# Performance work log

Hardware: AMD Instinct MI355X
Metric: run time of the kernel (lower is better)

## Reference

```python
import jax, jax.numpy as jnp
import numpy as np

N = 120000   # hits
K = 512      # non-noise objects (ids 1..K; id 0 = noise)
D = 8        # cluster-space dim
C = 6        # pid classes
Q_MIN = 1.0
NOISE_THR = 0
PAYLOAD_W = 1.0
EPS = 1e-9


def setup_inputs() -> dict:
    key = jax.random.key(0)
    ks = jax.random.split(key, 9)
    beta = jax.random.uniform(ks[0], (N,), dtype=jnp.float32) * 0.95 + 0.01  # keep arctanh finite
    x = jax.random.normal(ks[1], (N, D), dtype=jnp.float32)
    object_id = jax.random.randint(ks[2], (N,), 0, K + 1).astype(jnp.int32)
    # guarantee every object id (and noise id 0) appears at least once
    object_id = object_id.at[: K + 1].set(jnp.arange(K + 1, dtype=jnp.int32))
    energy = jax.random.normal(ks[3], (N,), dtype=jnp.float32)
    energy_per_hit = jax.random.normal(ks[4], (N,), dtype=jnp.float32)
    momentum = jax.random.normal(ks[5], (N, 3), dtype=jnp.float32)
    momentum_per_hit = jax.random.normal(ks[6], (N, 3), dtype=jnp.float32)
    pid_logits = jax.random.normal(ks[7], (N, C), dtype=jnp.float32)
    pid_per_hit = jax.random.randint(ks[8], (N,), 0, C).astype(jnp.int32)
    return dict(beta=beta, x=x, object_id=object_id, energy=energy,
                energy_per_hit=energy_per_hit, momentum=momentum,
                momentum_per_hit=momentum_per_hit, pid_logits=pid_logits,
                pid_per_hit=pid_per_hit)


def _oc_core(beta, x, object_id):
    """condensation_loss_tiger with weights=1, max_n_rep=0 (no repulsive sampling)."""
    oids = jnp.arange(1, K + 1, dtype=object_id.dtype)
    att_mask = object_id[:, None] == oids[None, :]              # [N, K]
    q = jnp.arctanh(beta) ** 2 + Q_MIN                          # [N]
    alphas = jnp.argmax(q[:, None] * att_mask, axis=0)          # [K] condensation points
    x_k = x[alphas]                                             # [K, D]
    q_k = q[alphas]                                             # [K]
    # squared euclidean distance via gemm (avoids [N,K,D] intermediate)
    d2 = (jnp.sum(x * x, axis=1)[:, None] + jnp.sum(x_k * x_k, axis=1)[None, :]
          - 2.0 * (x @ x_k.T))
    d2 = jnp.maximum(d2, 0.0)                                   # [N, K]
    dist = jnp.sqrt(jnp.maximum(d2, 1e-12))
    qw = q[:, None] * q_k[None, :]                              # [N, K]
    # attractive: per-object normalized by hits in object, then mean over objects
    att_norm = jnp.sum(att_mask, axis=0).astype(x.dtype)        # [K]
    v_att = jnp.sum(jnp.where(att_mask, qw * d2, 0.0) / (att_norm + EPS)[None, :]) / K
    # repulsive: hinge (1 - dist), normalized by n_hits not in object
    rep_mask = (~att_mask) & (dist < 1.0)
    n_rep_k = jnp.sum(~att_mask, axis=0).astype(x.dtype)        # [K]
    n_rep = jnp.sum(rep_mask)
    v_rep = jnp.sum(jnp.where(rep_mask, qw * (1.0 - dist), 0.0) / (n_rep_k + EPS)[None, :]) / K
    l_coward = jnp.mean(1.0 - beta[alphas])
    noise_m = (object_id <= NOISE_THR).astype(beta.dtype)
    l_noise = jnp.sum(beta * noise_m) / jnp.sum(noise_m)
    return v_att, v_rep, l_coward, l_noise, n_rep


def reference(beta, x, object_id, energy, energy_per_hit, momentum,
              momentum_per_hit, pid_logits, pid_per_hit):
    v_att, v_rep, l_coward, l_noise, n_rep = _oc_core(beta, x, object_id)
    oc_total = v_att + v_rep + l_coward + l_noise
    # payload losses on non-noise hits (masked means == F.*_loss on gathered rows)
    m = (object_id > NOISE_THR).astype(beta.dtype)              # [N]
    nm = jnp.sum(m)
    e_loss = jnp.sum((energy - energy_per_hit) ** 2 * m) / nm
    p_loss = jnp.sum((momentum - momentum_per_hit) ** 2 * m[:, None]) / (nm * momentum.shape[1])
    logp = jax.nn.log_softmax(pid_logits, axis=-1)              # [N, C]
    nll = -jnp.take_along_axis(logp, pid_per_hit[:, None], axis=1)[:, 0]
    pid_loss = jnp.sum(nll * m) / nm
    total = oc_total + PAYLOAD_W * (e_loss + p_loss + pid_loss)
    return (v_att, v_rep, l_coward, l_noise, n_rep.astype(jnp.float32),
            oc_total, e_loss, p_loss, pid_loss, total)
```

## Files before the change

kernel.cpp:

```cpp
#include <hip/hip_runtime.h>
#include <math.h>

#define KOBJ 512
#define KTW 8
#define TK 32
#define NTILE (KOBJ / TK)
#define HB 8
#define HCH (256 * HB)
#define MPREP 512
#define GGATH 16

typedef _Float16 half2_t __attribute__((ext_vector_type(2)));

__device__ __forceinline__ float wave_red_f(float v) {
  #pragma unroll
  for (int off = 32; off > 0; off >>= 1) v += __shfl_down(v, off, 64);
  return v;
}

__device__ __forceinline__ float q_of_beta(float b) {
  float a = 0.5f * __logf((1.f + b) / (1.f - b));
  return fmaf(a, a, 1.f);
}

__device__ __forceinline__ float dot8h(uint4 kx, const uint* y, float acc) {
#if __has_builtin(__builtin_amdgcn_fdot2)
  acc = __builtin_amdgcn_fdot2(__builtin_bit_cast(half2_t, y[0]),
                               __builtin_bit_cast(half2_t, kx.x), acc, false);
  acc = __builtin_amdgcn_fdot2(__builtin_bit_cast(half2_t, y[1]),
                               __builtin_bit_cast(half2_t, kx.y), acc, false);
  acc = __builtin_amdgcn_fdot2(__builtin_bit_cast(half2_t, y[2]),
                               __builtin_bit_cast(half2_t, kx.z), acc, false);
  acc = __builtin_amdgcn_fdot2(__builtin_bit_cast(half2_t, y[3]),
                               __builtin_bit_cast(half2_t, kx.w), acc, false);
#else
  const uint kk[4] = {kx.x, kx.y, kx.z, kx.w};
  #pragma unroll
  for (int c = 0; c < 4; c++) {
    half2_t a = __builtin_bit_cast(half2_t, y[c]);
    half2_t b = __builtin_bit_cast(half2_t, kk[c]);
    acc = fmaf((float)a.x, (float)b.x, acc);
    acc = fmaf((float)a.y, (float)b.y, acc);
  }
#endif
  return acc;
}

__global__ __launch_bounds__(256) void
k_prep(const float* __restrict__ beta, const int* __restrict__ oid,
       const float* __restrict__ energy, const float* __restrict__ eph,
       const float* __restrict__ mom, const float* __restrict__ mph,
       const float* __restrict__ logits, const int* __restrict__ pid,
       unsigned long long* __restrict__ amax_part,
       unsigned* __restrict__ cnt_part,
       float* __restrict__ scal_part, int n) {
  __shared__ unsigned long long lmax[KOBJ];
  __shared__ unsigned lcnt[KOBJ];
  for (int t = threadIdx.x; t < KOBJ; t += 256) { lmax[t] = 0ull; lcnt[t] = 0u; }
  __syncthreads();

  float e_t = 0.f, p_t = 0.f, pid_t = 0.f, noise_t = 0.f, ncnt = 0.f, mcnt = 0.f;
  for (int i = blockIdx.x * 256 + threadIdx.x; i < n; i += MPREP * 256) {
    float b = beta[i];
    int o = oid[i];
    if (o > 0) {
      float q = q_of_beta(b);
      unsigned long long key = ((unsigned long long)__float_as_uint(q) << 32)
                             | (unsigned long long)(unsigned)(~(unsigned)i);
      atomicMax(&lmax[o - 1], key);
      atomicAdd(&lcnt[o - 1], 1u);
      mcnt += 1.f;
      float de = energy[i] - eph[i];
      e_t = fmaf(de, de, e_t);
      float p0 = mom[3*i+0] - mph[3*i+0];
      float p1 = mom[3*i+1] - mph[3*i+1];
      float p2 = mom[3*i+2] - mph[3*i+2];
      p_t = fmaf(p0, p0, p_t); p_t = fmaf(p1, p1, p_t); p_t = fmaf(p2, p2, p_t);
      const float* lg = logits + 6*i;
      float l0=lg[0], l1=lg[1], l2=lg[2], l3=lg[3], l4=lg[4], l5=lg[5];
      float mx = fmaxf(fmaxf(fmaxf(l0,l1),fmaxf(l2,l3)), fmaxf(l4,l5));
      float s = __expf(l0-mx)+__expf(l1-mx)+__expf(l2-mx)
              + __expf(l3-mx)+__expf(l4-mx)+__expf(l5-mx);
      int pc = pid[i];
      float lp = (pc==0)?l0:(pc==1)?l1:(pc==2)?l2:(pc==3)?l3:(pc==4)?l4:l5;
      pid_t += mx + __logf(s) - lp;
    } else {
      noise_t += b;
      ncnt += 1.f;
    }
  }
  __syncthreads();

  for (int t = threadIdx.x; t < KOBJ; t += 256) {
    amax_part[(size_t)blockIdx.x * KOBJ + t] = lmax[t];
    cnt_part[(size_t)blockIdx.x * KOBJ + t]  = lcnt[t];
  }

  float vals[6] = {e_t, p_t, pid_t, noise_t, ncnt, mcnt};
  #pragma unroll
  for (int j = 0; j < 6; j++) vals[j] = wave_red_f(vals[j]);
  __shared__ float sred[4][6];
  int w = threadIdx.x >> 6, l = threadIdx.x & 63;
  if (l == 0) {
    #pragma unroll
    for (int j = 0; j < 6; j++) sred[w][j] = vals[j];
  }
  __syncthreads();
  if (threadIdx.x == 0) {
    #pragma unroll
    for (int j = 0; j < 6; j++)
      scal_part[blockIdx.x * 8 + j] = sred[0][j]+sred[1][j]+sred[2][j]+sred[3][j];
  }
}

__global__ __launch_bounds__(256) void
k_gather(const float* __restrict__ x, const float* __restrict__ beta,
         const unsigned long long* __restrict__ amax_part,
         const unsigned* __restrict__ cnt_part,
         uint* __restrict__ ktab, float* __restrict__ cow_part, int n) {
  int ko = threadIdx.x & 31;
  int chunk = threadIdx.x >> 5;
  int k = blockIdx.x * 32 + ko;
  const int mpc = MPREP / 8;
  int m0 = chunk * mpc, m1 = m0 + mpc;

  unsigned long long key = 0ull;
  unsigned cnt = 0u;
  for (int m = m0; m < m1; m++) {
    unsigned long long km = amax_part[(size_t)m * KOBJ + k];
    key = (km > key) ? km : key;
    cnt += cnt_part[(size_t)m * KOBJ + k];
  }
  __shared__ unsigned long long skey[8][32];
  __shared__ unsigned scnt[8][32];
  skey[chunk][ko] = key;
  scnt[chunk][ko] = cnt;
  __syncthreads();

  float cow = 0.f;
  if (chunk == 0) {
    #pragma unroll
    for (int c = 1; c < 8; c++) {
      unsigned long long kc = skey[c][ko];
      key = (kc > key) ? kc : key;
      cnt += scnt[c][ko];
    }
    unsigned idx = ~(unsigned)(key & 0xffffffffull);
    float q_k = __uint_as_float((unsigned)(key >> 32));
    const float4* xp = (const float4*)x;
    float4 xa = xp[2 * (size_t)idx];
    float4 xb = xp[2 * (size_t)idx + 1];
    float xv[8] = {xa.x, xa.y, xa.z, xa.w, xb.x, xb.y, xb.z, xb.w};
    float s2 = 0.f;
    #pragma unroll
    for (int c = 0; c < 8; c++) s2 = fmaf(xv[c], xv[c], s2);
    uint* kt = ktab + (size_t)k * KTW;
    #pragma unroll
    for (int c = 0; c < 4; c++) {
      half2_t hp = { (_Float16)xv[2*c], (_Float16)xv[2*c+1] };
      kt[c] = __builtin_bit_cast(uint, hp);
    }
    kt[4] = __float_as_uint(s2);
    kt[5] = __float_as_uint(q_k / ((float)(n - (int)cnt) + 1e-9f));
    kt[6] = __float_as_uint(q_k / ((float)cnt + 1e-9f));
    kt[7] = 0u;
    cow = 1.f - beta[idx];
  }
  cow = wave_red_f(cow);
  if (threadIdx.x == 0) cow_part[blockIdx.x] = cow;
}

__global__ __launch_bounds__(256, 4) void
k_pairs(const float* __restrict__ x, const float* __restrict__ beta,
        const int* __restrict__ oid, const uint* __restrict__ ktab,
        float* __restrict__ pairs_part, int n) {
  __shared__ __align__(16) uint skt[TK * KTW];
  const int tid = threadIdx.x;
  const int tile0 = blockIdx.y * TK;
  const int hbase = blockIdx.x * HCH;

  for (int t = tid; t < TK * KTW; t += 256)
    skt[t] = ktab[(size_t)tile0 * KTW + t];
  __syncthreads();

  uint yh[HB][4];
  float thr[HB], bh[HB], qi[HB];
  int own[HB];
  const float4* xp = (const float4*)x;
  #pragma unroll
  for (int h = 0; h < HB; h++) {
    int i = hbase + h * 256 + tid;
    if (i < n) {
      float4 xa = xp[2 * (size_t)i];
      float4 xb = xp[2 * (size_t)i + 1];
      float xi[8] = {xa.x, xa.y, xa.z, xa.w, xb.x, xb.y, xb.z, xb.w};
      float s = 0.f;
      #pragma unroll
      for (int c = 0; c < 8; c++) s = fmaf(xi[c], xi[c], s);
      bh[h] = s;
      thr[h] = 1.f - s;
      #pragma unroll
      for (int c = 0; c < 4; c++) {
        half2_t hy = { (_Float16)(-2.f * xi[2*c]), (_Float16)(-2.f * xi[2*c+1]) };
        yh[h][c] = __builtin_bit_cast(uint, hy);
      }
      qi[h] = q_of_beta(beta[i]);
      own[h] = oid[i] - 1 - tile0;
    } else {
      #pragma unroll
      for (int c = 0; c < 4; c++) yh[h][c] = 0u;
      bh[h] = 0.f;
      thr[h] = -1e30f;
      qi[h] = 0.f;
      own[h] = -1;
    }
  }

  float att = 0.f, rep = 0.f, nrep = 0.f;
  #pragma unroll 2
  for (int k = 0; k < TK; k++) {
    const uint* kr = &skt[k * KTW];
    uint4 kx = *(const uint4*)kr;
    float s2 = __uint_as_float(kr[4]);
    float wr = __uint_as_float(kr[5]);
    #pragma unroll
    for (int h = 0; h < HB; h++) {
      float dp = dot8h(kx, yh[h], s2);
      if (dp < thr[h]) {
        float d2 = dp + bh[h];
        float dist = sqrtf(fmaxf(d2, 1e-12f));
        rep = fmaf(qi[h] * (1.f - dist), wr, rep);
        nrep += 1.f;
      }
    }
  }

  #pragma unroll
  for (int h = 0; h < HB; h++) {
    int ko = own[h];
    if (ko >= 0 && ko < TK) {
      const uint* kr = &skt[ko * KTW];
      uint4 kx = *(const uint4*)kr;
      float s2 = __uint_as_float(kr[4]);
      float wr = __uint_as_float(kr[5]);
      float wa = __uint_as_float(kr[6]);
      float dp = dot8h(kx, yh[h], s2);
      float d2 = dp + bh[h];
      att = fmaf(qi[h] * fmaxf(d2, 0.f), wa, att);
      if (dp < thr[h]) {
        float dist = sqrtf(fmaxf(d2, 1e-12f));
        rep = fmaf(-qi[h] * (1.f - dist), wr, rep);
        nrep -= 1.f;
      }
    }
  }

  att = wave_red_f(att);
  rep = wave_red_f(rep);
  nrep = wave_red_f(nrep);
  __shared__ float sred[4][3];
  int w = tid >> 6, l = tid & 63;
  if (l == 0) { sred[w][0] = att; sred[w][1] = rep; sred[w][2] = nrep; }
  __syncthreads();
  if (tid == 0) {
    int bid = blockIdx.y * gridDim.x + blockIdx.x;
    pairs_part[bid * 4 + 0] = sred[0][0]+sred[1][0]+sred[2][0]+sred[3][0];
    pairs_part[bid * 4 + 1] = sred[0][1]+sred[1][1]+sred[2][1]+sred[3][1];
    pairs_part[bid * 4 + 2] = sred[0][2]+sred[1][2]+sred[2][2]+sred[3][2];
  }
}

__global__ __launch_bounds__(256) void
k_finalize(const float* __restrict__ pairs_part, int nblk_tot,
           const float* __restrict__ scal_part,
           const float* __restrict__ cow_part, float* __restrict__ out) {
  float v[9] = {0,0,0,0,0,0,0,0,0};
  for (int b = threadIdx.x; b < nblk_tot; b += 256) {
    v[0] += pairs_part[b * 4 + 0];
    v[1] += pairs_part[b * 4 + 1];
    v[2] += pairs_part[b * 4 + 2];
  }
  for (int m = threadIdx.x; m < MPREP; m += 256) {
    #pragma unroll
    for (int j = 0; j < 6; j++) v[3 + j] += scal_part[m * 8 + j];
  }
  #pragma unroll
  for (int j = 0; j < 9; j++) v[j] = wave_red_f(v[j]);
  __shared__ float sred[4][9];
  int w = threadIdx.x >> 6, l = threadIdx.x & 63;
  if (l == 0) {
    #pragma unroll
    for (int j = 0; j < 9; j++) sred[w][j] = v[j];
  }
  __syncthreads();
  if (threadIdx.x == 0) {
    float t[9];
    #pragma unroll
    for (int j = 0; j < 9; j++) t[j] = sred[0][j]+sred[1][j]+sred[2][j]+sred[3][j];
    float cow = 0.f;
    #pragma unroll
    for (int g = 0; g < GGATH; g++) cow += cow_part[g];
    float v_att  = t[0] / (float)KOBJ;
    float v_rep  = t[1] / (float)KOBJ;
    float n_rep  = t[2];
    float l_cow  = cow / (float)KOBJ;
    float l_noise = t[6] / t[7];
    float oc = v_att + v_rep + l_cow + l_noise;
    float nm = t[8];
    float e_loss  = t[3] / nm;
    float p_loss  = t[4] / (nm * 3.f);
    float pid_loss = t[5] / nm;
    out[0] = v_att;
    out[1] = v_rep;
    out[2] = l_cow;
    out[3] = l_noise;
    out[4] = n_rep;
    out[5] = oc;
    out[6] = e_loss;
    out[7] = p_loss;
    out[8] = pid_loss;
    out[9] = oc + e_loss + p_loss + pid_loss;
  }
}

extern "C" void kernel_launch(void* const* d_in, const int* in_sizes, int n_in,
                              void* d_out, int out_size, void* d_ws, size_t ws_size,
                              hipStream_t stream) {
  const float* beta   = (const float*)d_in[0];
  const float* x      = (const float*)d_in[1];
  const int*   oid    = (const int*)d_in[2];
  const float* energy = (const float*)d_in[3];
  const float* eph    = (const float*)d_in[4];
  const float* mom    = (const float*)d_in[5];
  const float* mph    = (const float*)d_in[6];
  const float* logits = (const float*)d_in[7];
  const int*   pid    = (const int*)d_in[8];
  float* out = (float*)d_out;
  const int n = in_sizes[0];
  const int nhb = (n + HCH - 1) / HCH;
  const int nblk_tot = nhb * NTILE;

  char* base = (char*)d_ws;
  size_t off = 0;
  uint*  ktab       = (uint*)(base + off);  off += (size_t)KOBJ * KTW * 4;
  float* cow_part   = (float*)(base + off); off += GGATH * 4;
  float* pairs_part = (float*)(base + off); off += (size_t)nblk_tot * 4 * 4;
  off = (off + 255) & ~(size_t)255;
  unsigned long long* amax_part = (unsigned long long*)(base + off); off += (size_t)MPREP * KOBJ * 8;
  unsigned* cnt_part = (unsigned*)(base + off);                      off += (size_t)MPREP * KOBJ * 4;
  float* scal_part   = (float*)(base + off);                         off += (size_t)MPREP * 8 * 4;

  k_prep<<<MPREP, 256, 0, stream>>>(beta, oid, energy, eph, mom, mph, logits, pid,
                                    amax_part, cnt_part, scal_part, n);
  k_gather<<<GGATH, 256, 0, stream>>>(x, beta, amax_part, cnt_part, ktab, cow_part, n);
  k_pairs<<<dim3(nhb, NTILE), 256, 0, stream>>>(x, beta, oid, ktab, pairs_part, n);
  k_finalize<<<1, 256, 0, stream>>>(pairs_part, nblk_tot, scal_part, cow_part, out);
}
```

Before: 114.7 us.

## Fuse gather, pairs and finalize into one kernel with last-block reduction

Removes the separate gather and finalize launches. Each pairs block now reduces the per-block argmax and count partials for its own object tile and builds the tile table in shared memory. The last block to finish, found through an atomic counter, does the final reduction. The prep grid is cut to 128 blocks so that each main block has fewer partials to reduce, at the cost of less parallelism in prep. Every main block now repeats the tile's partial reduction, which adds redundant global reads.

```diff
diff --git a/kernel.cpp b/kernel.cpp
--- a/kernel.cpp
+++ b/kernel.cpp
@@ -7,10 +7,12 @@
 #define NTILE (KOBJ / TK)
 #define HB 8
 #define HCH (256 * HB)
-#define MPREP 512
-#define GGATH 16
+#define MPREP 128
 
 typedef _Float16 half2_t __attribute__((ext_vector_type(2)));
+
+#define AGS(p, v) __hip_atomic_store((p), (v), __ATOMIC_RELAXED, __HIP_MEMORY_SCOPE_AGENT)
+#define AGL(p)    __hip_atomic_load((p), __ATOMIC_RELAXED, __HIP_MEMORY_SCOPE_AGENT)
 
 __device__ __forceinline__ float wave_red_f(float v) {
   #pragma unroll
@@ -53,9 +55,11 @@
        const float* __restrict__ logits, const int* __restrict__ pid,
        unsigned long long* __restrict__ amax_part,
        unsigned* __restrict__ cnt_part,
-       float* __restrict__ scal_part, int n) {
+       float* __restrict__ scal_part,
+       unsigned* __restrict__ done_cnt, int n) {
   __shared__ unsigned long long lmax[KOBJ];
   __shared__ unsigned lcnt[KOBJ];
+  if (blockIdx.x == 0 && threadIdx.x == 0) *done_cnt = 0u;
   for (int t = threadIdx.x; t < KOBJ; t += 256) { lmax[t] = 0ull; lcnt[t] = 0u; }
   __syncthreads();
 
@@ -113,78 +117,76 @@
   }
 }
 
-__global__ __launch_bounds__(256) void
-k_gather(const float* __restrict__ x, const float* __restrict__ beta,
-         const unsigned long long* __restrict__ amax_part,
-         const unsigned* __restrict__ cnt_part,
-         uint* __restrict__ ktab, float* __restrict__ cow_part, int n) {
-  int ko = threadIdx.x & 31;
-  int chunk = threadIdx.x >> 5;
-  int k = blockIdx.x * 32 + ko;
-  const int mpc = MPREP / 8;
-  int m0 = chunk * mpc, m1 = m0 + mpc;
-
-  unsigned long long key = 0ull;
-  unsigned cnt = 0u;
-  for (int m = m0; m < m1; m++) {
-    unsigned long long km = amax_part[(size_t)m * KOBJ + k];
-    key = (km > key) ? km : key;
-    cnt += cnt_part[(size_t)m * KOBJ + k];
-  }
+__global__ __launch_bounds__(256, 4) void
+k_main(const float* __restrict__ x, const float* __restrict__ beta,
+       const int* __restrict__ oid,
+       const unsigned long long* __restrict__ amax_part,
+       const unsigned* __restrict__ cnt_part,
+       const float* __restrict__ scal_part,
+       float* __restrict__ cow_part, float* __restrict__ pairs_part,
+       unsigned* __restrict__ done_cnt, float* __restrict__ out, int n) {
+  __shared__ __align__(16) uint skt[TK * KTW];
   __shared__ unsigned long long skey[8][32];
-  __shared__ unsigned scnt[8][32];
-  skey[chunk][ko] = key;
-  scnt[chunk][ko] = cnt;
-  __syncthreads();
-
-  float cow = 0.f;
-  if (chunk == 0) {
-    #pragma unroll
-    for (int c = 1; c < 8; c++) {
-      unsigned long long kc = skey[c][ko];
-      key = (kc > key) ? kc : key;
-      cnt += scnt[c][ko];
-    }
-    unsigned idx = ~(unsigned)(key & 0xffffffffull);
-    float q_k = __uint_as_float((unsigned)(key >> 32));
-    const float4* xp = (const float4*)x;
-    float4 xa = xp[2 * (size_t)idx];
-    float4 xb = xp[2 * (size_t)idx + 1];
-    float xv[8] = {xa.x, xa.y, xa.z, xa.w, xb.x, xb.y, xb.z, xb.w};
-    float s2 = 0.f;
-    #pragma unroll
-    for (int c = 0; c < 8; c++) s2 = fmaf(xv[c], xv[c], s2);
-    uint* kt = ktab + (size_t)k * KTW;
-    #pragma unroll
-    for (int c = 0; c < 4; c++) {
-      half2_t hp = { (_Float16)xv[2*c], (_Float16)xv[2*c+1] };
-      kt[c] = __builtin_bit_cast(uint, hp);
-    }
-    kt[4] = __float_as_uint(s2);
-    kt[5] = __float_as_uint(q_k / ((float)(n - (int)cnt) + 1e-9f));
-    kt[6] = __float_as_uint(q_k / ((float)cnt + 1e-9f));
-    kt[7] = 0u;
-    cow = 1.f - beta[idx];
-  }
-  cow = wave_red_f(cow);
-  if (threadIdx.x == 0) cow_part[blockIdx.x] = cow;
-}
-
-__global__ __launch_bounds__(256, 4) void
-k_pairs(const float* __restrict__ x, const float* __restrict__ beta,
-        const int* __restrict__ oid, const uint* __restrict__ ktab,
-        float* __restrict__ pairs_part, int n) {
-  __shared__ __align__(16) uint skt[TK * KTW];
+  __shared__ unsigned scnt_s[8][32];
+  __shared__ float sredu[4][10];
+  __shared__ unsigned slast;
+
   const int tid = threadIdx.x;
+  const int w = tid >> 6, l = tid & 63;
   const int tile0 = blockIdx.y * TK;
   const int hbase = blockIdx.x * HCH;
-
-  for (int t = tid; t < TK * KTW; t += 256)
-    skt[t] = ktab[(size_t)tile0 * KTW + t];
-  __syncthreads();
+  const int nblk = gridDim.x * gridDim.y;
+  const int bid = blockIdx.y * gridDim.x + blockIdx.x;
+
+  {
+    int ko = tid & 31, seg = tid >> 5;
+    unsigned long long key = 0ull;
+    unsigned cnt = 0u;
+    for (int m = seg; m < MPREP; m += 8) {
+      unsigned long long km = amax_part[(size_t)m * KOBJ + tile0 + ko];
+      key = (km > key) ? km : key;
+      cnt += cnt_part[(size_t)m * KOBJ + tile0 + ko];
+    }
+    skey[seg][ko] = key;
+    scnt_s[seg][ko] = cnt;
+    __syncthreads();
+    float cowv = 0.f;
+    if (tid < 32) {
+      #pragma unroll
+      for (int c = 1; c < 8; c++) {
+        unsigned long long kc = skey[c][tid];
+        key = (kc > key) ? kc : key;
+        cnt += scnt_s[c][tid];
+      }
+      unsigned idx = ~(unsigned)(key & 0xffffffffull);
+      float q_k = __uint_as_float((unsigned)(key >> 32));
+      const float4* xp4 = (const float4*)x;
+      float4 xa = xp4[2 * (size_t)idx];
+      float4 xb = xp4[2 * (size_t)idx + 1];
+      float xv[8] = {xa.x, xa.y, xa.z, xa.w, xb.x, xb.y, xb.z, xb.w};
+      float s2 = 0.f;
+      #pragma unroll
+      for (int c = 0; c < 8; c++) s2 = fmaf(xv[c], xv[c], s2);
+      uint* kt = &skt[tid * KTW];
+      #pragma unroll
+      for (int c = 0; c < 4; c++) {
+        half2_t hp = { (_Float16)xv[2*c], (_Float16)xv[2*c+1] };
+        kt[c] = __builtin_bit_cast(uint, hp);
+      }
+      kt[4] = __float_as_uint(s2);
+      kt[5] = __float_as_uint(q_k / ((float)(n - (int)cnt) + 1e-9f));
+      kt[6] = __float_as_uint(q_k / ((float)cnt + 1e-9f));
+      if (blockIdx.x == 0) cowv = 1.f - beta[idx];
+    }
+    if (tid < 64) {
+      cowv = wave_red_f(cowv);
+      if (tid == 0 && blockIdx.x == 0) AGS(&cow_part[blockIdx.y], cowv);
+    }
+    __syncthreads();
+  }
 
   uint yh[HB][4];
-  float thr[HB], bh[HB], qi[HB];
+  float thr[HB], bh2[HB], qi[HB];
   int own[HB];
   const float4* xp = (const float4*)x;
   #pragma unroll
@@ -197,7 +199,7 @@
       float s = 0.f;
       #pragma unroll
       for (int c = 0; c < 8; c++) s = fmaf(xi[c], xi[c], s);
-      bh[h] = s;
+      bh2[h] = s;
       thr[h] = 1.f - s;
       #pragma unroll
       for (int c = 0; c < 4; c++) {
@@ -209,7 +211,7 @@
     } else {
       #pragma unroll
       for (int c = 0; c < 4; c++) yh[h][c] = 0u;
-      bh[h] = 0.f;
+      bh2[h] = 0.f;
       thr[h] = -1e30f;
       qi[h] = 0.f;
       own[h] = -1;
@@ -218,8 +220,8 @@
 
   float att = 0.f, rep = 0.f, nrep = 0.f;
   #pragma unroll 2
-  for (int k = 0; k < TK; k++) {
-    const uint* kr = &skt[k * KTW];
+  for (int k2 = 0; k2 < TK; k2++) {
+    const uint* kr = &skt[k2 * KTW];
     uint4 kx = *(const uint4*)kr;
     float s2 = __uint_as_float(kr[4]);
     float wr = __uint_as_float(kr[5]);
@@ -227,7 +229,7 @@
     for (int h = 0; h < HB; h++) {
       float dp = dot8h(kx, yh[h], s2);
       if (dp < thr[h]) {
-        float d2 = dp + bh[h];
+        float d2 = dp + bh2[h];
         float dist = sqrtf(fmaxf(d2, 1e-12f));
         rep = fmaf(qi[h] * (1.f - dist), wr, rep);
         nrep += 1.f;
@@ -245,7 +247,7 @@
       float wr = __uint_as_float(kr[5]);
       float wa = __uint_as_float(kr[6]);
       float dp = dot8h(kx, yh[h], s2);
-      float d2 = dp + bh[h];
+      float d2 = dp + bh2[h];
       att = fmaf(qi[h] * fmaxf(d2, 0.f), wa, att);
       if (dp < thr[h]) {
         float dist = sqrtf(fmaxf(d2, 1e-12f));
@@ -258,68 +260,63 @@
   att = wave_red_f(att);
   rep = wave_red_f(rep);
   nrep = wave_red_f(nrep);
-  __shared__ float sred[4][3];
-  int w = tid >> 6, l = tid & 63;
-  if (l == 0) { sred[w][0] = att; sred[w][1] = rep; sred[w][2] = nrep; }
+  if (l == 0) { sredu[w][0] = att; sredu[w][1] = rep; sredu[w][2] = nrep; }
   __syncthreads();
   if (tid == 0) {
-    int bid = blockIdx.y * gridDim.x + blockIdx.x;
-    pairs_part[bid * 4 + 0] = sred[0][0]+sred[1][0]+sred[2][0]+sred[3][0];
-    pairs_part[bid * 4 + 1] = sred[0][1]+sred[1][1]+sred[2][1]+sred[3][1];
-    pairs_part[bid * 4 + 2] = sred[0][2]+sred[1][2]+sred[2][2]+sred[3][2];
-  }
-}
-
-__global__ __launch_bounds__(256) void
-k_finalize(const float* __restrict__ pairs_part, int nblk_tot,
-           const float* __restrict__ scal_part,
-           const float* __restrict__ cow_part, float* __restrict__ out) {
-  float v[9] = {0,0,0,0,0,0,0,0,0};
-  for (int b = threadIdx.x; b < nblk_tot; b += 256) {
-    v[0] += pairs_part[b * 4 + 0];
-    v[1] += pairs_part[b * 4 + 1];
-    v[2] += pairs_part[b * 4 + 2];
-  }
-  for (int m = threadIdx.x; m < MPREP; m += 256) {
+    AGS(&pairs_part[bid * 4 + 0], sredu[0][0]+sredu[1][0]+sredu[2][0]+sredu[3][0]);
+    AGS(&pairs_part[bid * 4 + 1], sredu[0][1]+sredu[1][1]+sredu[2][1]+sredu[3][1]);
+    AGS(&pairs_part[bid * 4 + 2], sredu[0][2]+sredu[1][2]+sredu[2][2]+sredu[3][2]);
+    slast = __hip_atomic_fetch_add(done_cnt, 1u, __ATOMIC_ACQ_REL,
+                                   __HIP_MEMORY_SCOPE_AGENT);
+  }
+  __syncthreads();
+
+  if (slast == (unsigned)(nblk - 1)) {
+    float v[10] = {0,0,0,0,0,0,0,0,0,0};
+    for (int b2 = tid; b2 < nblk; b2 += 256) {
+      v[0] += AGL(&pairs_part[b2 * 4 + 0]);
+      v[1] += AGL(&pairs_part[b2 * 4 + 1]);
+      v[2] += AGL(&pairs_part[b2 * 4 + 2]);
+    }
+    for (int m = tid; m < MPREP; m += 256) {
+      #pragma unroll
+      for (int j = 0; j < 6; j++) v[3 + j] += scal_part[m * 8 + j];
+    }
+    for (int g = tid; g < NTILE; g += 256) v[9] += AGL(&cow_part[g]);
     #pragma unroll
-    for (int j = 0; j < 6; j++) v[3 + j] += scal_part[m * 8 + j];
-  }
-  #pragma unroll
-  for (int j = 0; j < 9; j++) v[j] = wave_red_f(v[j]);
-  __shared__ float sred[4][9];
-  int w = threadIdx.x >> 6, l = threadIdx.x & 63;
-  if (l == 0) {
-    #pragma unroll
-    for (int j = 0; j < 9; j++) sred[w][j] = v[j];
-  }
-  __syncthreads();
-  if (threadIdx.x == 0) {
-    float t[9];
-    #pragma unroll
-    for (int j = 0; j < 9; j++) t[j] = sred[0][j]+sred[1][j]+sred[2][j]+sred[3][j];
-    float cow = 0.f;
-    #pragma unroll
-    for (int g = 0; g < GGATH; g++) cow += cow_part[g];
-    float v_att  = t[0] / (float)KOBJ;
-    float v_rep  = t[1] / (float)KOBJ;
-    float n_rep  = t[2];
-    float l_cow  = cow / (float)KOBJ;
-    float l_noise = t[6] / t[7];
-    float oc = v_att + v_rep + l_cow + l_noise;
-    float nm = t[8];
-    float e_loss  = t[3] / nm;
-    float p_loss  = t[4] / (nm * 3.f);
-    float pid_loss = t[5] / nm;
-    out[0] = v_att;
-    out[1] = v_rep;
-    out[2] = l_cow;
-    out[3] = l_noise;
-    out[4] = n_rep;
-    out[5] = oc;
-    out[6] = e_loss;
-    out[7] = p_loss;
-    out[8] = pid_loss;
-    out[9] = oc + e_loss + p_loss + pid_loss;
+    for (int j = 0; j < 10; j++) v[j] = wave_red_f(v[j]);
+    __syncthreads();
+    if (l == 0) {
+      #pragma unroll
+      for (int j = 0; j < 10; j++) sredu[w][j] = v[j];
+    }
+    __syncthreads();
+    if (tid == 0) {
+      float t10[10];
+      #pragma unroll
+      for (int j = 0; j < 10; j++)
+        t10[j] = sredu[0][j]+sredu[1][j]+sredu[2][j]+sredu[3][j];
+      float v_att  = t10[0] / (float)KOBJ;
+      float v_rep  = t10[1] / (float)KOBJ;
+      float n_rep  = t10[2];
+      float l_cow  = t10[9] / (float)KOBJ;
+      float l_noise = t10[6] / t10[7];
+      float oc = v_att + v_rep + l_cow + l_noise;
+      float nm = t10[8];
+      float e_loss  = t10[3] / nm;
+      float p_loss  = t10[4] / (nm * 3.f);
+      float pid_loss = t10[5] / nm;
+      out[0] = v_att;
+      out[1] = v_rep;
+      out[2] = l_cow;
+      out[3] = l_noise;
+      out[4] = n_rep;
+      out[5] = oc;
+      out[6] = e_loss;
+      out[7] = p_loss;
+      out[8] = pid_loss;
+      out[9] = oc + e_loss + p_loss + pid_loss;
+    }
   }
 }
 
@@ -335,24 +332,24 @@
   const float* mph    = (const float*)d_in[6];
   const float* logits = (const float*)d_in[7];
   const int*   pid    = (const int*)d_in[8];
-  float* out = (float*)d_out;
+  float* outp = (float*)d_out;
   const int n = in_sizes[0];
   const int nhb = (n + HCH - 1) / HCH;
   const int nblk_tot = nhb * NTILE;
 
   char* base = (char*)d_ws;
   size_t off = 0;
-  uint*  ktab       = (uint*)(base + off);  off += (size_t)KOBJ * KTW * 4;
-  float* cow_part   = (float*)(base + off); off += GGATH * 4;
+  float* cow_part   = (float*)(base + off); off += (size_t)NTILE * 4;
   float* pairs_part = (float*)(base + off); off += (size_t)nblk_tot * 4 * 4;
+  float* scal_part  = (float*)(base + off); off += (size_t)MPREP * 8 * 4;
+  unsigned* done_cnt = (unsigned*)(base + off); off += 256;
   off = (off + 255) & ~(size_t)255;
   unsigned long long* amax_part = (unsigned long long*)(base + off); off += (size_t)MPREP * KOBJ * 8;
   unsigned* cnt_part = (unsigned*)(base + off);                      off += (size_t)MPREP * KOBJ * 4;
-  float* scal_part   = (float*)(base + off);                         off += (size_t)MPREP * 8 * 4;
 
   k_prep<<<MPREP, 256, 0, stream>>>(beta, oid, energy, eph, mom, mph, logits, pid,
-                                    amax_part, cnt_part, scal_part, n);
-  k_gather<<<GGATH, 256, 0, stream>>>(x, beta, amax_part, cnt_part, ktab, cow_part, n);
-  k_pairs<<<dim3(nhb, NTILE), 256, 0, stream>>>(x, beta, oid, ktab, pairs_part, n);
-  k_finalize<<<1, 256, 0, stream>>>(pairs_part, nblk_tot, scal_part, cow_part, out);
-}
+                                    amax_part, cnt_part, scal_part, done_cnt, n);
+  k_main<<<dim3(nhb, NTILE), 256, 0, stream>>>(x, beta, oid, amax_part, cnt_part,
+                                               scal_part, cow_part, pairs_part,
+                                               done_cnt, outp, n);
+}
```

Result: slower. 121.2 us (+5.7%).
